# Optimization experiments

Hardware: AMD Instinct MI355X
Metric: run time of the kernel (lower is better)

The kernel has to match this reference:

```python
import jax, jax.numpy as jnp
import numpy as np

C = 64
HW = 21 * 21  # 441
NEIGHBOR_K = 3


def setup_inputs() -> dict:
    key = jax.random.key(0)
    k1, k2, k3, k4 = jax.random.split(key, 4)
    B1, B2 = 32, 25
    x1 = jax.random.normal(k1, (B1, C, 21, 21), dtype=jnp.float32)
    x2 = jax.random.normal(k2, (B2, C, 21, 21), dtype=jnp.float32)
    mask1 = jax.random.uniform(k3, (B1, 21, 21), dtype=jnp.float32)
    mask2 = jax.random.uniform(k4, (B2, 21, 21), dtype=jnp.float32)
    return {"x1": x1, "x2": x2, "mask1": mask1, "mask2": mask2}


def reference(x1, x2, mask1, mask2):
    B1 = x1.shape[0]
    B2 = x2.shape[0]
    q = x1.reshape(B1, C, HW)  # (B1, 64, 441) query descriptors
    s = x2.reshape(B2, C, HW)  # (B2, 64, 441) support descriptors
    # per-descriptor L2 norms over channel dim
    qn = jnp.linalg.norm(q, axis=1)  # (B1, 441)
    sn = jnp.linalg.norm(s, axis=1)  # (B2, 441)
    # cosine similarity between every query descriptor and every support descriptor
    inner = jnp.einsum('aci,bcj->abij', q, s)  # (B1, B2, 441, 441)
    sim = inner / (qn[:, None, :, None] * sn[None, :, None, :])
    # mask out invalid spatial positions on both sides
    sim = sim * mask1.reshape(B1, 1, HW, 1) * mask2.reshape(1, B2, 1, HW)
    # top-k nearest support descriptors per query descriptor, sum over all
    topk_vals, _ = jax.lax.top_k(sim, NEIGHBOR_K)  # (B1, B2, 441, k)
    return topk_vals.reshape(B1, B2, -1).sum(axis=2)  # (B1, B2)
```

## Files before the change

kernel.cpp:

```cpp
#include <hip/hip_runtime.h>
#include <math.h>

#define CCH 64
#define HW 441
#define HWP 448
#define NT 28
#define NB2 25
#define PANEL (HWP * CCH)
#define NI 4

typedef _Float16 half8 __attribute__((ext_vector_type(8)));
typedef __fp16 h2 __attribute__((ext_vector_type(2)));
typedef float f32x4 __attribute__((ext_vector_type(4)));

__global__ __launch_bounds__(64) void normalize_frag_kernel(
        const float* __restrict__ x1, const float* __restrict__ m1,
        const float* __restrict__ x2, const float* __restrict__ m2,
        _Float16* __restrict__ qh, _Float16* __restrict__ sh,
        float* __restrict__ out, int nout, int n1rows, int nrows) {
    int idx = blockIdx.x * blockDim.x + threadIdx.x;
    if (idx < nout) out[idx] = 0.f;
    if (idx >= nrows) return;
    const float* x; const float* mk; _Float16* outp; int rb;
    if (idx < n1rows) { x = x1; mk = m1; outp = qh; rb = idx; }
    else             { x = x2; mk = m2; outp = sh; rb = idx - n1rows; }
    int b = rb / HWP, i = rb - b * HWP;
    float vals[CCH];
    if (i < HW) {
        const float* xb = x + (size_t)b * CCH * HW + i;
        float ss = 0.f;
#pragma unroll
        for (int c = 0; c < CCH; ++c) { float v = xb[c * HW]; vals[c] = v; ss += v * v; }
        float scale = mk[b * HW + i] * rsqrtf(ss);
#pragma unroll
        for (int c = 0; c < CCH; ++c) vals[c] *= scale;
    } else {
#pragma unroll
        for (int c = 0; c < CCH; ++c) vals[c] = 0.f;
    }
    _Float16* pb = outp + (size_t)b * PANEL + (i >> 4) * 1024 + (i & 15) * 8;
#pragma unroll
    for (int f = 0; f < 2; ++f) {
#pragma unroll
        for (int qd = 0; qd < 4; ++qd) {
            half8 h;
#pragma unroll
            for (int e = 0; e < 8; ++e) h[e] = (_Float16)vals[f * 32 + qd * 8 + e];
            *(half8*)(pb + f * 512 + qd * 128) = h;
        }
    }
}

static __device__ __forceinline__ h2 hmax2(h2 a, h2 b) {
    return __builtin_elementwise_max(a, b);
}
static __device__ __forceinline__ h2 hmin2(h2 a, h2 b) {
    return __builtin_elementwise_min(a, b);
}

#define PK_INSERT(v, p0, p1, p2)           \
    do {                                   \
        h2 _m = hmax2(p0, v);              \
        h2 _c = hmin2(p0, v);              \
        p0 = _m;                           \
        _m = hmax2(p1, _c);                \
        _c = hmin2(p1, _c);                \
        p1 = _m;                           \
        p2 = hmax2(p2, _c);                \
    } while (0)

#define MERGE3(t0, t1, t2, b0, b1, b2)            \
    do {                                          \
        float _m0 = fmaxf(t0, b0);                \
        float _n0 = fminf(t0, b0);                \
        float _m1 = fmaxf(t1, b1);                \
        float _t2 = fmaxf(t2, b2);                \
        t0 = _m0;                                 \
        t1 = fmaxf(_n0, _m1);                     \
        t2 = fmaxf(fminf(_n0, _m1), _t2);         \
    } while (0)

template <bool MASKED>
__device__ __forceinline__ void do_pass_j(const _Float16* __restrict__ qtiles,
                                          const _Float16* __restrict__ spanel,
                                          int jt0, int nfull, int lane, int quad,
                                          float (&t0)[NI], float (&t1)[NI], float (&t2)[NI]) {
    const float NEG = -1e30f;
    const f32x4 FZ = {0.f, 0.f, 0.f, 0.f};
    const h2 NEGH = {(__fp16)-65504.f, (__fp16)-65504.f};
    half8 bf0[NI], bf1[NI];
#pragma unroll
    for (int t = 0; t < NI; ++t) {
        const _Float16* qp = qtiles + t * 1024 + lane * 8;
        bf0[t] = *(const half8*)qp;
        bf1[t] = *(const half8*)(qp + 512);
    }
    h2 p0[NI], p1[NI], p2[NI];
#pragma unroll
    for (int t = 0; t < NI; ++t) { p0[t] = NEGH; p1[t] = NEGH; p2[t] = NEGH; }

    const _Float16* sp = spanel + (size_t)jt0 * 1024 + lane * 8;
    half8 c0 = *(const half8*)sp;
    half8 c1 = *(const half8*)(sp + 512);

    for (int jt = 0; jt < nfull; ++jt) {
        int nx = (jt + 1 < nfull + (MASKED ? 1 : 0)) ? jt + 1 : jt;
        const _Float16* np = sp + (size_t)nx * 1024;
        half8 n0 = *(const half8*)np;
        half8 n1 = *(const half8*)(np + 512);
#pragma unroll
        for (int t = 0; t < NI; ++t) {
            f32x4 z = __builtin_amdgcn_mfma_f32_16x16x32_f16(c0, bf0[t], FZ, 0, 0, 0);
            z = __builtin_amdgcn_mfma_f32_16x16x32_f16(c1, bf1[t], z, 0, 0, 0);
            h2 c02 = __builtin_amdgcn_cvt_pkrtz(z[0], z[2]);
            h2 c13 = __builtin_amdgcn_cvt_pkrtz(z[1], z[3]);
            PK_INSERT(c02, p0[t], p1[t], p2[t]);
            PK_INSERT(c13, p0[t], p1[t], p2[t]);
        }
        c0 = n0; c1 = n1;
    }
    if (MASKED) {
#pragma unroll
        for (int t = 0; t < NI; ++t) {
            f32x4 z = __builtin_amdgcn_mfma_f32_16x16x32_f16(c0, bf0[t], FZ, 0, 0, 0);
            z = __builtin_amdgcn_mfma_f32_16x16x32_f16(c1, bf1[t], z, 0, 0, 0);
#pragma unroll
            for (int r = 0; r < 4; ++r)
                if (quad * 4 + r >= 9) z[r] = NEG;
            h2 c02 = __builtin_amdgcn_cvt_pkrtz(z[0], z[2]);
            h2 c13 = __builtin_amdgcn_cvt_pkrtz(z[1], z[3]);
            PK_INSERT(c02, p0[t], p1[t], p2[t]);
            PK_INSERT(c13, p0[t], p1[t], p2[t]);
        }
    }

#pragma unroll
    for (int t = 0; t < NI; ++t) {
        float a0 = (float)p0[t][0], a1 = (float)p1[t][0], a2 = (float)p2[t][0];
        float b0 = (float)p0[t][1], b1 = (float)p1[t][1], b2 = (float)p2[t][1];
        MERGE3(a0, a1, a2, b0, b1, b2);
        b0 = __shfl_xor(a0, 16); b1 = __shfl_xor(a1, 16); b2 = __shfl_xor(a2, 16);
        MERGE3(a0, a1, a2, b0, b1, b2);
        b0 = __shfl_xor(a0, 32); b1 = __shfl_xor(a1, 32); b2 = __shfl_xor(a2, 32);
        MERGE3(a0, a1, a2, b0, b1, b2);
        t0[t] = a0; t1[t] = a1; t2[t] = a2;
    }
}

__global__ __launch_bounds__(128, 4) void sim_topk_mfma(const _Float16* __restrict__ qh,
                                                        const _Float16* __restrict__ sh,
                                                        float* __restrict__ out) {
    __shared__ float s_tri[2][NI][16][3];
    int blk = blockIdx.x;
    int pair = blk / 7, g = blk - pair * 7;
    int a = pair / NB2, b = pair - a * NB2;
    int tid = threadIdx.x, wave = tid >> 6, lane = tid & 63;
    int m = lane & 15, quad = lane >> 4;
    const _Float16* qtiles = qh + (size_t)a * PANEL + (size_t)g * NI * 1024;
    const _Float16* spanel = sh + (size_t)b * PANEL;

    float t0[NI], t1[NI], t2[NI];
    if (wave == 0)
        do_pass_j<false>(qtiles, spanel, 0, 14, lane, quad, t0, t1, t2);
    else
        do_pass_j<true>(qtiles, spanel, 14, 13, lane, quad, t0, t1, t2);

    if (quad == 0) {
#pragma unroll
        for (int t = 0; t < NI; ++t) {
            s_tri[wave][t][m][0] = t0[t];
            s_tri[wave][t][m][1] = t1[t];
            s_tri[wave][t][m][2] = t2[t];
        }
    }
    __syncthreads();

    if (wave == 0) {
        int t = quad;
        float a0 = s_tri[0][t][m][0], a1 = s_tri[0][t][m][1], a2 = s_tri[0][t][m][2];
        float b0 = s_tri[1][t][m][0], b1 = s_tri[1][t][m][1], b2 = s_tri[1][t][m][2];
        MERGE3(a0, a1, a2, b0, b1, b2);
        float r = a0 + a1 + a2;
#pragma unroll
        for (int off = 32; off > 0; off >>= 1) r += __shfl_down(r, off);
        if (lane == 0) atomicAdd(&out[pair], r);
    }
}

extern "C" void kernel_launch(void* const* d_in, const int* in_sizes, int n_in,
                              void* d_out, int out_size, void* d_ws, size_t ws_size,
                              hipStream_t stream) {
    const float* x1 = (const float*)d_in[0];
    const float* x2 = (const float*)d_in[1];
    const float* m1 = (const float*)d_in[2];
    const float* m2 = (const float*)d_in[3];
    float* out = (float*)d_out;

    int B1 = in_sizes[0] / (CCH * HW);
    int B2 = in_sizes[1] / (CCH * HW);

    _Float16* qh = (_Float16*)d_ws;
    _Float16* sh = qh + (size_t)B1 * PANEL;

    int n1 = B1 * HWP, ntot = (B1 + B2) * HWP;
    normalize_frag_kernel<<<(ntot + 63) / 64, 64, 0, stream>>>(
        x1, m1, x2, m2, qh, sh, out, B1 * B2, n1, ntot);
    sim_topk_mfma<<<B1 * B2 * 7, 128, 0, stream>>>(qh, sh, out);
}
```

Baseline: 98.58 us.

## Switch similarity tiles to 32x32x16 MFMA with a single j-pass per wave

Repacks the normalized half-precision panels into 32-row tiles so that each wave issues 32x32x16 MFMAs over the full support panel, instead of four 16x16 query tiles with the support range split between two waves. Each wave now owns one 32-query tile and runs the whole top-3 scan itself, which removes the shared-memory merge and the block barrier. The launch-bounds occupancy hint rises from 4 to 5. In exchange, each lane holds 16 accumulators per MFMA, the inner loop is serial over 14 tiles per wave, and the last tile is masked to row 12 only in the lower half.

```diff
diff --git a/kernel.cpp b/kernel.cpp
--- a/kernel.cpp
+++ b/kernel.cpp
@@ -4,14 +4,14 @@
 #define CCH 64
 #define HW 441
 #define HWP 448
-#define NT 28
 #define NB2 25
 #define PANEL (HWP * CCH)
-#define NI 4
+#define TSTR 2048
+#define NJT 14
 
 typedef _Float16 half8 __attribute__((ext_vector_type(8)));
 typedef __fp16 h2 __attribute__((ext_vector_type(2)));
-typedef float f32x4 __attribute__((ext_vector_type(4)));
+typedef float f32x16 __attribute__((ext_vector_type(16)));
 
 __global__ __launch_bounds__(64) void normalize_frag_kernel(
         const float* __restrict__ x1, const float* __restrict__ m1,
@@ -38,15 +38,15 @@
 #pragma unroll
         for (int c = 0; c < CCH; ++c) vals[c] = 0.f;
     }
-    _Float16* pb = outp + (size_t)b * PANEL + (i >> 4) * 1024 + (i & 15) * 8;
+    _Float16* pb = outp + (size_t)b * PANEL + (size_t)(i >> 5) * TSTR + (i & 31) * 8;
 #pragma unroll
-    for (int f = 0; f < 2; ++f) {
+    for (int f = 0; f < 4; ++f) {
 #pragma unroll
-        for (int qd = 0; qd < 4; ++qd) {
+        for (int hh = 0; hh < 2; ++hh) {
             half8 h;
 #pragma unroll
-            for (int e = 0; e < 8; ++e) h[e] = (_Float16)vals[f * 32 + qd * 8 + e];
-            *(half8*)(pb + f * 512 + qd * 128) = h;
+            for (int e = 0; e < 8; ++e) h[e] = (_Float16)vals[f * 16 + hh * 8 + e];
+            *(half8*)(pb + f * 512 + hh * 256) = h;
         }
     }
 }
@@ -80,111 +80,80 @@
         t2 = fmaxf(fminf(_n0, _m1), _t2);         \
     } while (0)
 
-template <bool MASKED>
-__device__ __forceinline__ void do_pass_j(const _Float16* __restrict__ qtiles,
-                                          const _Float16* __restrict__ spanel,
-                                          int jt0, int nfull, int lane, int quad,
-                                          float (&t0)[NI], float (&t1)[NI], float (&t2)[NI]) {
-    const float NEG = -1e30f;
-    const f32x4 FZ = {0.f, 0.f, 0.f, 0.f};
-    const h2 NEGH = {(__fp16)-65504.f, (__fp16)-65504.f};
-    half8 bf0[NI], bf1[NI];
-#pragma unroll
-    for (int t = 0; t < NI; ++t) {
-        const _Float16* qp = qtiles + t * 1024 + lane * 8;
-        bf0[t] = *(const half8*)qp;
-        bf1[t] = *(const half8*)(qp + 512);
-    }
-    h2 p0[NI], p1[NI], p2[NI];
-#pragma unroll
-    for (int t = 0; t < NI; ++t) { p0[t] = NEGH; p1[t] = NEGH; p2[t] = NEGH; }
+#define MFMA32(z, c, q) z = __builtin_amdgcn_mfma_f32_32x32x16_f16(c, q, z, 0, 0, 0)
 
-    const _Float16* sp = spanel + (size_t)jt0 * 1024 + lane * 8;
-    half8 c0 = *(const half8*)sp;
-    half8 c1 = *(const half8*)(sp + 512);
-
-    for (int jt = 0; jt < nfull; ++jt) {
-        int nx = (jt + 1 < nfull + (MASKED ? 1 : 0)) ? jt + 1 : jt;
-        const _Float16* np = sp + (size_t)nx * 1024;
-        half8 n0 = *(const half8*)np;
-        half8 n1 = *(const half8*)(np + 512);
-#pragma unroll
-        for (int t = 0; t < NI; ++t) {
-            f32x4 z = __builtin_amdgcn_mfma_f32_16x16x32_f16(c0, bf0[t], FZ, 0, 0, 0);
-            z = __builtin_amdgcn_mfma_f32_16x16x32_f16(c1, bf1[t], z, 0, 0, 0);
-            h2 c02 = __builtin_amdgcn_cvt_pkrtz(z[0], z[2]);
-            h2 c13 = __builtin_amdgcn_cvt_pkrtz(z[1], z[3]);
-            PK_INSERT(c02, p0[t], p1[t], p2[t]);
-            PK_INSERT(c13, p0[t], p1[t], p2[t]);
-        }
-        c0 = n0; c1 = n1;
-    }
-    if (MASKED) {
-#pragma unroll
-        for (int t = 0; t < NI; ++t) {
-            f32x4 z = __builtin_amdgcn_mfma_f32_16x16x32_f16(c0, bf0[t], FZ, 0, 0, 0);
-            z = __builtin_amdgcn_mfma_f32_16x16x32_f16(c1, bf1[t], z, 0, 0, 0);
-#pragma unroll
-            for (int r = 0; r < 4; ++r)
-                if (quad * 4 + r >= 9) z[r] = NEG;
-            h2 c02 = __builtin_amdgcn_cvt_pkrtz(z[0], z[2]);
-            h2 c13 = __builtin_amdgcn_cvt_pkrtz(z[1], z[3]);
-            PK_INSERT(c02, p0[t], p1[t], p2[t]);
-            PK_INSERT(c13, p0[t], p1[t], p2[t]);
-        }
-    }
-
-#pragma unroll
-    for (int t = 0; t < NI; ++t) {
-        float a0 = (float)p0[t][0], a1 = (float)p1[t][0], a2 = (float)p2[t][0];
-        float b0 = (float)p0[t][1], b1 = (float)p1[t][1], b2 = (float)p2[t][1];
-        MERGE3(a0, a1, a2, b0, b1, b2);
-        b0 = __shfl_xor(a0, 16); b1 = __shfl_xor(a1, 16); b2 = __shfl_xor(a2, 16);
-        MERGE3(a0, a1, a2, b0, b1, b2);
-        b0 = __shfl_xor(a0, 32); b1 = __shfl_xor(a1, 32); b2 = __shfl_xor(a2, 32);
-        MERGE3(a0, a1, a2, b0, b1, b2);
-        t0[t] = a0; t1[t] = a1; t2[t] = a2;
-    }
-}
-
-__global__ __launch_bounds__(128, 4) void sim_topk_mfma(const _Float16* __restrict__ qh,
+__global__ __launch_bounds__(128, 5) void sim_topk_mfma(const _Float16* __restrict__ qh,
                                                         const _Float16* __restrict__ sh,
                                                         float* __restrict__ out) {
-    __shared__ float s_tri[2][NI][16][3];
     int blk = blockIdx.x;
     int pair = blk / 7, g = blk - pair * 7;
     int a = pair / NB2, b = pair - a * NB2;
     int tid = threadIdx.x, wave = tid >> 6, lane = tid & 63;
-    int m = lane & 15, quad = lane >> 4;
-    const _Float16* qtiles = qh + (size_t)a * PANEL + (size_t)g * NI * 1024;
-    const _Float16* spanel = sh + (size_t)b * PANEL;
+    int hi = lane >> 5;
+    const float NEG = -1e30f;
+    const h2 NEGH = {(__fp16)-65504.f, (__fp16)-65504.f};
 
-    float t0[NI], t1[NI], t2[NI];
-    if (wave == 0)
-        do_pass_j<false>(qtiles, spanel, 0, 14, lane, quad, t0, t1, t2);
-    else
-        do_pass_j<true>(qtiles, spanel, 14, 13, lane, quad, t0, t1, t2);
+    const _Float16* qt = qh + (size_t)a * PANEL + (size_t)(g * 2 + wave) * TSTR + lane * 8;
+    half8 qf0 = *(const half8*)(qt);
+    half8 qf1 = *(const half8*)(qt + 512);
+    half8 qf2 = *(const half8*)(qt + 1024);
+    half8 qf3 = *(const half8*)(qt + 1536);
 
-    if (quad == 0) {
+    const _Float16* sp = sh + (size_t)b * PANEL + lane * 8;
+    half8 c0 = *(const half8*)(sp);
+    half8 c1 = *(const half8*)(sp + 512);
+    half8 c2 = *(const half8*)(sp + 1024);
+    half8 c3 = *(const half8*)(sp + 1536);
+
+    h2 p0 = NEGH, p1 = NEGH, p2 = NEGH;
+
+    for (int jt = 0; jt < NJT - 1; ++jt) {
+        const _Float16* np = sp + (size_t)(jt + 1) * TSTR;
+        half8 n0 = *(const half8*)(np);
+        half8 n1 = *(const half8*)(np + 512);
+        half8 n2 = *(const half8*)(np + 1024);
+        half8 n3 = *(const half8*)(np + 1536);
+
+        f32x16 z = {0.f, 0.f, 0.f, 0.f, 0.f, 0.f, 0.f, 0.f,
+                    0.f, 0.f, 0.f, 0.f, 0.f, 0.f, 0.f, 0.f};
+        MFMA32(z, c0, qf0);
+        MFMA32(z, c1, qf1);
+        MFMA32(z, c2, qf2);
+        MFMA32(z, c3, qf3);
 #pragma unroll
-        for (int t = 0; t < NI; ++t) {
-            s_tri[wave][t][m][0] = t0[t];
-            s_tri[wave][t][m][1] = t1[t];
-            s_tri[wave][t][m][2] = t2[t];
+        for (int r = 0; r < 8; ++r) {
+            h2 c = __builtin_amdgcn_cvt_pkrtz(z[2 * r], z[2 * r + 1]);
+            PK_INSERT(c, p0, p1, p2);
         }
+        c0 = n0; c1 = n1; c2 = n2; c3 = n3;
     }
-    __syncthreads();
 
-    if (wave == 0) {
-        int t = quad;
-        float a0 = s_tri[0][t][m][0], a1 = s_tri[0][t][m][1], a2 = s_tri[0][t][m][2];
-        float b0 = s_tri[1][t][m][0], b1 = s_tri[1][t][m][1], b2 = s_tri[1][t][m][2];
-        MERGE3(a0, a1, a2, b0, b1, b2);
-        float r = a0 + a1 + a2;
+    {
+        f32x16 z = {0.f, 0.f, 0.f, 0.f, 0.f, 0.f, 0.f, 0.f,
+                    0.f, 0.f, 0.f, 0.f, 0.f, 0.f, 0.f, 0.f};
+        MFMA32(z, c0, qf0);
+        MFMA32(z, c1, qf1);
+        MFMA32(z, c2, qf2);
+        MFMA32(z, c3, qf3);
 #pragma unroll
-        for (int off = 32; off > 0; off >>= 1) r += __shfl_down(r, off);
-        if (lane == 0) atomicAdd(&out[pair], r);
+        for (int r = 0; r < 6; ++r) {
+            h2 c = __builtin_amdgcn_cvt_pkrtz(z[2 * r], z[2 * r + 1]);
+            PK_INSERT(c, p0, p1, p2);
+        }
+        float z12 = hi ? NEG : z[12];
+        h2 c = __builtin_amdgcn_cvt_pkrtz(z12, NEG);
+        PK_INSERT(c, p0, p1, p2);
     }
+
+    float a0 = (float)p0[0], a1 = (float)p1[0], a2 = (float)p2[0];
+    float b0 = (float)p0[1], b1 = (float)p1[1], b2 = (float)p2[1];
+    MERGE3(a0, a1, a2, b0, b1, b2);
+    b0 = __shfl_xor(a0, 32); b1 = __shfl_xor(a1, 32); b2 = __shfl_xor(a2, 32);
+    MERGE3(a0, a1, a2, b0, b1, b2);
+    float rsum = hi ? 0.f : (a0 + a1 + a2);
+#pragma unroll
+    for (int off = 32; off > 0; off >>= 1) rsum += __shfl_xor(rsum, off);
+    if (lane == 0) atomicAdd(&out[pair], rsum);
 }
 
 extern "C" void kernel_launch(void* const* d_in, const int* in_sizes, int n_in,
```

New measurement: 101.2 us. +2.6%, slower.
